# Kernel optimization log

Hardware: AMD Instinct MI355X
Metric: run time of the kernel (lower is better)

## Reference

```python
import jax, jax.numpy as jnp
import numpy as np

B, N, D_MODEL = 2, 2048, 1024
H, HEAD_DIM, D1 = 16, 128, 2048
NK, RANK = 16, 32
GAMMA = 0.999


def setup_inputs() -> dict:
    key = jax.random.key(0)
    ks = jax.random.split(key, 12)
    std = 0.02
    return {
        "x": jax.random.normal(ks[0], (B, N, D_MODEL), jnp.float32),
        "Wu": jax.random.normal(ks[1], (D_MODEL, D1), jnp.float32) * std,
        "bu": jax.random.normal(ks[2], (D1,), jnp.float32) * std,
        "Wv": jax.random.normal(ks[3], (D_MODEL, D1), jnp.float32) * std,
        "bv": jax.random.normal(ks[4], (D1,), jnp.float32) * std,
        "Wo": jax.random.normal(ks[5], (D1, D_MODEL), jnp.float32) * std,
        "bo": jax.random.normal(ks[6], (D_MODEL,), jnp.float32) * std,
        # SKI low-rank Toeplitz kernel factors at nk inducing relative positions
        "a_pos": jax.random.normal(ks[7], (H, NK, RANK), jnp.float32) * 0.1,
        "b_pos": jax.random.normal(ks[8], (H, RANK, HEAD_DIM), jnp.float32) * 0.1,
        "a_neg": jax.random.normal(ks[9], (H, NK, RANK), jnp.float32) * 0.1,
        "b_neg": jax.random.normal(ks[10], (H, RANK, HEAD_DIM), jnp.float32) * 0.1,
        "t_zero": jax.random.normal(ks[11], (H, HEAD_DIM), jnp.float32) * 0.1,
    }


def _interp_decay_kernel(a, b, n):
    # low-rank kernel at nk inducing points: [h, nk, d]
    k_ind = jnp.einsum("hkr,hrd->hkd", a, b)
    lags = jnp.arange(1, n)                      # lags 1..n-1
    p = (lags - 1.0) / (n - 2.0) * (NK - 1)      # map lag onto inducing grid
    lo = jnp.floor(p).astype(jnp.int32)
    hi = jnp.minimum(lo + 1, NK - 1)
    w = (p - lo)[None, :, None]
    k = k_ind[:, lo, :] * (1.0 - w) + k_ind[:, hi, :] * w  # [h, n-1, d]
    decay = (GAMMA ** lags)[None, :, None]
    return k * decay


def reference(x, Wu, bu, Wv, bv, Wo, bo, a_pos, b_pos, a_neg, b_neg, t_zero):
    u = jax.nn.silu(x @ Wu + bu)                 # [b, n, d1]
    v = jax.nn.silu(x @ Wv + bv)                 # [b, n, d1]
    n = v.shape[1]
    vh = v.reshape(v.shape[0], n, H, HEAD_DIM)   # [b, n, h, d]

    kp = _interp_decay_kernel(a_pos, b_pos, n)   # [h, n-1, d]
    kn = _interp_decay_kernel(a_neg, b_neg, n)   # [h, n-1, d]
    m = 2 * n
    k_full = jnp.zeros((H, m, HEAD_DIM), vh.dtype)
    k_full = k_full.at[:, 0].set(t_zero)
    k_full = k_full.at[:, 1:n].set(kp)
    k_full = k_full.at[:, m - jnp.arange(1, n)].set(kn)  # non-causal (negative lags)

    # circular FFT convolution along the sequence axis
    vf = jnp.fft.rfft(vh, n=m, axis=1)                    # [b, mf, h, d]
    kf = jnp.transpose(jnp.fft.rfft(k_full, axis=1), (1, 0, 2))[None]  # [1, mf, h, d]
    y = jnp.fft.irfft(vf * kf, n=m, axis=1)[:, :n]        # [b, n, h, d]

    out = u * y.reshape(y.shape[0], n, D1)                # elementwise gate
    return out @ Wo + bo
```

## Files before the change

### kernel.cpp

```cpp
#include <hip/hip_runtime.h>
#include <hip/hip_bf16.h>
#include <stdint.h>
#include <stddef.h>

#define BB 2
#define NSEQ 2048
#define DM 1024
#define H 16
#define HD 128
#define D1 2048
#define NKI 16
#define RANKI 32
#define MROWS (BB * NSEQ)
#define VPROWS 6144
#define NTAP 28
#define NPAIR 13
#define NCHUNK 128
#define CLEN 16
#define NSEG 16
#define SEGC (NCHUNK / NSEG)
#define GAMMA_F 0.999f
#define G_CL 0.9841201f
#define G_SC8 0.87979895f
#define LN_G (-1.00050033e-3f)

__device__ constexpr int TAPS[NTAP] = {
  1, 2, 138, 139, 274, 275, 411, 412, 547, 548, 684,
  820, 821, 956, 957, 1093, 1094, 1229, 1230, 1366,
  1502, 1503, 1638, 1639, 1775, 1776, 1911, 1912};
__device__ constexpr int LEADL[NPAIR] = {1, 138, 274, 411, 547, 820, 956, 1093, 1229, 1502, 1638, 1775, 1911};
__device__ constexpr int LEADI[NPAIR] = {0, 2, 4, 6, 8, 11, 13, 15, 17, 20, 22, 24, 26};
#define SGL0_L 684
#define SGL0_I 10
#define SGL1_L 1366
#define SGL1_I 19

typedef short short8 __attribute__((ext_vector_type(8)));
typedef float floatx4 __attribute__((ext_vector_type(4)));

__device__ __forceinline__ float bf2f(unsigned short u) {
  union { unsigned int i; float f; } v; v.i = ((unsigned int)u) << 16; return v.f;
}
__device__ __forceinline__ unsigned short f2bf(float f) {
  union { float f; unsigned int i; } v; v.f = f;
  unsigned int r = (v.i + 0x7FFFu + ((v.i >> 16) & 1u)) >> 16;
  return (unsigned short)r;
}
__device__ __forceinline__ float bflo(unsigned int p) {
  union { unsigned int i; float f; } v; v.i = p << 16; return v.f;
}
__device__ __forceinline__ float bfhi(unsigned int p) {
  union { unsigned int i; float f; } v; v.i = p & 0xffff0000u; return v.f;
}
__device__ __forceinline__ void async16(const unsigned short* g, unsigned short* l) {
  __builtin_amdgcn_global_load_lds(
      (const __attribute__((address_space(1))) unsigned int*)g,
      (__attribute__((address_space(3))) unsigned int*)l, 16, 0, 0);
}

#define CVT4 (MROWS * DM / 4)
__global__ __launch_bounds__(256) void prep_kernel(const float* __restrict__ x,
                                                   unsigned short* __restrict__ x_bf,
                                                   unsigned short* __restrict__ zrow) {
  int i = blockIdx.x * 256 + threadIdx.x;
  if (i < CVT4) {
    float4 f = ((const float4*)x)[i];
    ushort4 o;
    o.x = f2bf(f.x); o.y = f2bf(f.y); o.z = f2bf(f.z); o.w = f2bf(f.w);
    ((ushort4*)x_bf)[i] = o;
  } else {
    int j = i - CVT4;
    if (j < 256) {
      uint4 z; z.x = z.y = z.z = z.w = 0u;
      ((uint4*)zrow)[j] = z;
    }
  }
}

__device__ __forceinline__ float KinterpL(const float* kk, int l, int d) {
  if (l < 1) return 0.0f;
  float p = (float)(l - 1) * (15.0f / 2046.0f);
  int lo = (int)p; if (lo > 15) lo = 15;
  int hi = lo + 1; if (hi > 15) hi = 15;
  float w = p - (float)lo;
  float v = kk[lo * HD + d] * (1.0f - w) + kk[hi * HD + d] * w;
  return v * __powf(GAMMA_F, (float)l);
}

__global__ __launch_bounds__(256) void wprep_kernel(const float* __restrict__ Wu,
                                                    const float* __restrict__ Wv,
                                                    const float* __restrict__ Wo,
                                                    unsigned short* __restrict__ WT2,
                                                    unsigned short* __restrict__ WoT,
                                                    const float* __restrict__ ap,
                                                    const float* __restrict__ bp,
                                                    const float* __restrict__ an,
                                                    const float* __restrict__ bn,
                                                    float* __restrict__ dtp,
                                                    float* __restrict__ dtn) {
  int blk = blockIdx.x;
  int tid = threadIdx.x;
  if (blk < 6144) {
    __shared__ unsigned short t[32][33];
    const float* in; unsigned short* out;
    int rows, cols, bx, by;
    if (blk < 2048) {
      in = Wo; out = WoT; rows = D1; cols = DM;
      bx = (blk & 31) * 32; by = (blk >> 5) * 32;
    } else {
      int local = blk - 2048;
      int z = local >> 11, l2 = local & 2047;
      in = z ? Wv : Wu; out = WT2 + (size_t)z * D1 * DM;
      rows = DM; cols = D1;
      bx = (l2 & 63) * 32; by = (l2 >> 6) * 32;
    }
    int tx = tid & 31, ty = tid >> 5;
#pragma unroll
    for (int j = 0; j < 32; j += 8)
      t[ty + j][tx] = f2bf(in[(size_t)(by + ty + j) * cols + bx + tx]);
    __syncthreads();
#pragma unroll
    for (int j = 0; j < 32; j += 8)
      out[(size_t)(bx + ty + j) * rows + by + tx] = t[tx][ty + j];
  } else {
    __shared__ float kk[NKI * HD];
    int e0 = blk - 6144;
    int h = e0 & 15, dir = e0 >> 4;
    const float* a = (dir ? an : ap) + h * NKI * RANKI;
    const float* b = (dir ? bn : bp) + h * RANKI * HD;
    for (int e = tid; e < NKI * HD; e += 256) {
      int k = e >> 7, d = e & 127;
      float s = 0.0f;
#pragma unroll
      for (int r = 0; r < RANKI; ++r) s += a[k * RANKI + r] * b[r * HD + d];
      kk[e] = s;
    }
    __syncthreads();
    float* dt = (dir ? dtn : dtp) + (size_t)h * NTAP * HD;
    for (int e = tid; e < NTAP * HD; e += 256) {
      int j = e >> 7, d = e & 127;
      int l = TAPS[j];
      float K0 = KinterpL(kk, l, d);
      float K1 = KinterpL(kk, l - 1, d);
      float K2 = KinterpL(kk, l - 2, d);
      dt[e] = K0 - 2.0f * GAMMA_F * K1 + (GAMMA_F * GAMMA_F) * K2;
    }
  }
}

__global__ __launch_bounds__(512) void gemm_uv8(const unsigned short* __restrict__ A,
                                                const unsigned short* __restrict__ Bt,
                                                const float* __restrict__ bu,
                                                const float* __restrict__ bv,
                                                unsigned short* __restrict__ U,
                                                unsigned short* __restrict__ Vp) {
  __shared__ unsigned short lds[65536];
  constexpr int K = DM;
  constexpr int NT = K / 64;
  int lin = blockIdx.y * 16 + blockIdx.x;
  int swz = (lin & 7) * 32 + (lin >> 3);
  int n0 = (swz & 15) * 256;
  int m0 = (swz >> 4) * 256;
  int tid = threadIdx.x;
  int lane = tid & 63, w = tid >> 6;
  int wm = w >> 2, wn = w & 3;
  int q = lane >> 4, l16 = lane & 15;
  int srow = lane >> 3;
  int soff = ((lane & 7) ^ srow) << 3;
  const unsigned short* Ab = A + (size_t)(m0 + w * 8 + srow) * K + soff;
  const unsigned short* Bb = Bt + (size_t)(n0 + w * 8 + srow) * K + soff;
  unsigned aoff0 = w * 512;
  unsigned boff0 = 32768u + w * 512;
  int swk0 = (q ^ (l16 & 7)) << 3;
  int swk1 = ((4 | q) ^ (l16 & 7)) << 3;
  int pAr = wm * 8192;
  int pBr = 32768 + (wn >> 1) * 8192;
  int rB0 = (wn & 1) * 64;

  floatx4 acc[8][4];
#pragma unroll
  for (int f = 0; f < 8; ++f)
#pragma unroll
    for (int g = 0; g < 4; ++g) acc[f][g] = (floatx4){0.f, 0.f, 0.f, 0.f};

  auto stage = [&](int p, int t) {
    const unsigned short* a = Ab + t * 64;
    const unsigned short* b = Bb + t * 64;
    unsigned ao = aoff0 + p * 16384;
    unsigned bo = boff0 + p * 16384;
    async16(a,               &lds[ao]);
    async16(a + (size_t)64 * K,  &lds[ao + 4096]);
    async16(a + (size_t)128 * K, &lds[ao + 8192]);
    async16(a + (size_t)192 * K, &lds[ao + 12288]);
    async16(b,               &lds[bo]);
    async16(b + (size_t)64 * K,  &lds[bo + 4096]);
    async16(b + (size_t)128 * K, &lds[bo + 8192]);
    async16(b + (size_t)192 * K, &lds[bo + 12288]);
  };

  stage(0, 0);
  stage(1, 1);
  asm volatile("s_waitcnt vmcnt(8)" ::: "memory");
  __builtin_amdgcn_s_barrier();

  for (int t = 0; t < NT; ++t) {
    int p = t & 1;
    const unsigned short* As = &lds[pAr + p * 16384];
    const unsigned short* Bs = &lds[pBr + p * 16384];
    short8 bfr[4][2];
#pragma unroll
    for (int g = 0; g < 4; ++g) {
      int rh = (rB0 + g * 16 + l16) * 64;
      bfr[g][0] = *(const short8*)(Bs + rh + swk0);
      bfr[g][1] = *(const short8*)(Bs + rh + swk1);
    }
#pragma unroll
    for (int mh = 0; mh < 2; ++mh) {
      short8 af[4][2];
#pragma unroll
      for (int f = 0; f < 4; ++f) {
        int rh = ((mh * 4 + f) * 16 + l16) * 64;
        af[f][0] = *(const short8*)(As + rh + swk0);
        af[f][1] = *(const short8*)(As + rh + swk1);
      }
      __builtin_amdgcn_s_setprio(1);
#pragma unroll
      for (int f = 0; f < 4; ++f)
#pragma unroll
        for (int g = 0; g < 4; ++g) {
          acc[mh * 4 + f][g] = __builtin_amdgcn_mfma_f32_16x16x32_bf16(
              af[f][0], bfr[g][0], acc[mh * 4 + f][g], 0, 0, 0);
          acc[mh * 4 + f][g] = __builtin_amdgcn_mfma_f32_16x16x32_bf16(
              af[f][1], bfr[g][1], acc[mh * 4 + f][g], 0, 0, 0);
        }
      __builtin_amdgcn_s_setprio(0);
    }
    if (t == NT - 1) break;
    asm volatile("" ::: "memory");
    __builtin_amdgcn_s_barrier();
    if (t + 2 < NT) {
      stage(p, t + 2);
      asm volatile("s_waitcnt vmcnt(8)" ::: "memory");
    } else {
      asm volatile("s_waitcnt vmcnt(0)" ::: "memory");
    }
    __builtin_amdgcn_s_barrier();
  }

  int isv = (n0 >= 2048);
  const float* bias = isv ? bv : bu;
#pragma unroll
  for (int f = 0; f < 8; ++f) {
#pragma unroll
    for (int g = 0; g < 4; ++g) {
      int n = n0 + wn * 64 + g * 16 + l16;
      int nc = isv ? (n - 2048) : n;
      float bsv = bias[nc];
#pragma unroll
      for (int r = 0; r < 4; ++r) {
        int m = m0 + wm * 128 + f * 16 + q * 4 + r;
        float val = acc[f][g][r] + bsv;
        val = val / (1.0f + __expf(-val));
        if (isv) {
          size_t mrow = (size_t)(2048 + m + ((m >> 11) << 12));
          Vp[mrow * 2048 + nc] = f2bf(val);
        } else {
          U[(size_t)m * 2048 + nc] = f2bf(val);
        }
      }
    }
  }
}

__global__ __launch_bounds__(512) void gemm_out2(const unsigned short* __restrict__ A,
                                                 const unsigned short* __restrict__ Bt,
                                                 const float* __restrict__ bias,
                                                 float* __restrict__ C) {
  __shared__ unsigned short lds[32768];
  constexpr int K = D1;
  constexpr int NT = K / 64;
  int lin = blockIdx.y * 8 + blockIdx.x;
  int swz = (lin & 7) * 32 + (lin >> 3);
  int n0 = (swz & 7) * 128;
  int m0 = (swz >> 3) * 128;
  int tid = threadIdx.x;
  int lane = tid & 63, w = tid >> 6;
  int wm = w >> 1, wn = w & 1;
  int q = lane >> 4, l16 = lane & 15;
  int srow = lane >> 3;
  int soff = ((lane & 7) ^ srow) << 3;
  const unsigned short* Ab = A + (size_t)(m0 + w * 8 + srow) * K + soff;
  const unsigned short* Bb = Bt + (size_t)(n0 + w * 8 + srow) * K + soff;
  unsigned aoff0 = w * 512;
  unsigned boff0 = 16384u + w * 512;
  int swk0 = (q ^ (l16 & 7)) << 3;
  int swk1 = ((4 | q) ^ (l16 & 7)) << 3;

  floatx4 acc[2][4];
#pragma unroll
  for (int f = 0; f < 2; ++f)
#pragma unroll
    for (int g = 0; g < 4; ++g) acc[f][g] = (floatx4){0.f, 0.f, 0.f, 0.f};

  auto stage = [&](int p, int t) {
    const unsigned short* a = Ab + t * 64;
    const unsigned short* b = Bb + t * 64;
    unsigned ao = aoff0 + p * 8192;
    unsigned bo = boff0 + p * 8192;
    async16(a,                  &lds[ao]);
    async16(a + (size_t)64 * K, &lds[ao + 4096]);
    async16(b,                  &lds[bo]);
    async16(b + (size_t)64 * K, &lds[bo + 4096]);
  };

  stage(0, 0);
  stage(1, 1);
  asm volatile("s_waitcnt vmcnt(4)" ::: "memory");
  __builtin_amdgcn_s_barrier();

  for (int t = 0; t < NT; ++t) {
    int p = t & 1;
    const unsigned short* As = &lds[p * 8192];
    const unsigned short* Bs = &lds[16384 + p * 8192];
    short8 af[2][2], bfr[4][2];
#pragma unroll
    for (int g = 0; g < 4; ++g) {
      int rh = (wn * 64 + g * 16 + l16) * 64;
      bfr[g][0] = *(const short8*)(Bs + rh + swk0);
      bfr[g][1] = *(const short8*)(Bs + rh + swk1);
    }
#pragma unroll
    for (int f = 0; f < 2; ++f) {
      int rh = (wm * 32 + f * 16 + l16) * 64;
      af[f][0] = *(const short8*)(As + rh + swk0);
      af[f][1] = *(const short8*)(As + rh + swk1);
    }
    __builtin_amdgcn_s_setprio(1);
#pragma unroll
    for (int f = 0; f < 2; ++f)
#pragma unroll
      for (int g = 0; g < 4; ++g) {
        acc[f][g] = __builtin_amdgcn_mfma_f32_16x16x32_bf16(
            af[f][0], bfr[g][0], acc[f][g], 0, 0, 0);
        acc[f][g] = __builtin_amdgcn_mfma_f32_16x16x32_bf16(
            af[f][1], bfr[g][1], acc[f][g], 0, 0, 0);
      }
    __builtin_amdgcn_s_setprio(0);
    if (t == NT - 1) break;
    asm volatile("" ::: "memory");
    __builtin_amdgcn_s_barrier();
    if (t + 2 < NT) {
      stage(p, t + 2);
      asm volatile("s_waitcnt vmcnt(4)" ::: "memory");
    } else {
      asm volatile("s_waitcnt vmcnt(0)" ::: "memory");
    }
    __builtin_amdgcn_s_barrier();
  }

#pragma unroll
  for (int f = 0; f < 2; ++f) {
#pragma unroll
    for (int g = 0; g < 4; ++g) {
      int n = n0 + wn * 64 + g * 16 + l16;
      float bsv = bias[n];
#pragma unroll
      for (int r = 0; r < 4; ++r) {
        int m = m0 + wm * 32 + f * 16 + q * 4 + r;
        C[(size_t)m * DM + n] = acc[f][g][r] + bsv;
      }
    }
  }
}

__global__ __launch_bounds__(256, 1) void scan_chunks(const unsigned short* __restrict__ Vp,
                                                      const unsigned short* __restrict__ zr,
                                                      const float* __restrict__ dp,
                                                      const float* __restrict__ dn,
                                                      unsigned short* __restrict__ ypl,
                                                      unsigned short* __restrict__ ynl,
                                                      float* __restrict__ Sy_ex,
                                                      float* __restrict__ SG_ex) {
  int z = blockIdx.z;
  int dir = z >> 1, b = z & 1;
  int chunk = blockIdx.y;
  int c0 = blockIdx.x * 512 + threadIdx.x * 2;
  int h = c0 >> 7, d = c0 & 127;
  const float* dt = (dir ? dn : dp) + ((size_t)h * NTAP) * HD + d;
  float2 dreg[NTAP];
#pragma unroll
  for (int j = 0; j < NTAP; ++j) dreg[j] = *(const float2*)(dt + j * HD);
  const unsigned short* Vd = Vp + (size_t)b * VPROWS * D1 + (size_t)2048 * D1;
  unsigned short* yl = (dir ? ynl : ypl) + (size_t)b * NSEQ * D1 + c0;
  float sy0 = 0.f, sy1 = 0.f, sg0 = 0.f, sg1 = 0.f;
  float carry0[NPAIR], carry1[NPAIR];
  if (!dir) {
    int t0 = chunk * CLEN;
#pragma unroll
    for (int p = 0; p < NPAIR; ++p) {
      int tr = t0 - 1 - LEADL[p];
      const unsigned short* rb = (tr >= 0) ? (Vd + (size_t)tr * D1) : zr;
      unsigned int pk = *(const unsigned int*)(rb + c0);
      carry0[p] = bflo(pk); carry1[p] = bfhi(pk);
    }
    for (int i = 0; i < CLEN; ++i) {
      int t = t0 + i;
      float F0 = 0.f, F1 = 0.f;
#pragma unroll
      for (int p = 0; p < NPAIR; ++p) {
        int tr = t - LEADL[p];
        const unsigned short* rb = (tr >= 0) ? (Vd + (size_t)tr * D1) : zr;
        unsigned int pk = *(const unsigned int*)(rb + c0);
        float vl0 = bflo(pk), vl1 = bfhi(pk);
        F0 += dreg[LEADI[p]].x * vl0 + dreg[LEADI[p] + 1].x * carry0[p];
        F1 += dreg[LEADI[p]].y * vl1 + dreg[LEADI[p] + 1].y * carry1[p];
        carry0[p] = vl0; carry1[p] = vl1;
      }
      {
        int tr = t - SGL0_L;
        const unsigned short* rb = (tr >= 0) ? (Vd + (size_t)tr * D1) : zr;
        unsigned int pk = *(const unsigned int*)(rb + c0);
        F0 += dreg[SGL0_I].x * bflo(pk); F1 += dreg[SGL0_I].y * bfhi(pk);
      }
      {
        int tr = t - SGL1_L;
        const unsigned short* rb = (tr >= 0) ? (Vd + (size_t)tr * D1) : zr;
        unsigned int pk = *(const unsigned int*)(rb + c0);
        F0 += dreg[SGL1_I].x * bflo(pk); F1 += dreg[SGL1_I].y * bfhi(pk);
      }
      sg0 = GAMMA_F * sg0 + F0; sy0 = GAMMA_F * sy0 + sg0;
      sg1 = GAMMA_F * sg1 + F1; sy1 = GAMMA_F * sy1 + sg1;
      unsigned int pack = (unsigned int)f2bf(sy0) | ((unsigned int)f2bf(sy1) << 16);
      *(unsigned int*)(yl + (size_t)t * D1) = pack;
    }
  } else {
    int tstart = (NSEQ - 1) - chunk * CLEN;
#pragma unroll
    for (int p = 0; p < NPAIR; ++p) {
      int tr = tstart + 1 + LEADL[p];
      const unsigned short* rb = (tr <= NSEQ - 1) ? (Vd + (size_t)tr * D1) : zr;
      unsigned int pk = *(const unsigned int*)(rb + c0);
      carry0[p] = bflo(pk); carry1[p] = bfhi(pk);
    }
    for (int i = 0; i < CLEN; ++i) {
      int t = tstart - i;
      float F0 = 0.f, F1 = 0.f;
#pragma unroll
      for (int p = 0; p < NPAIR; ++p) {
        int tr = t + LEADL[p];
        const unsigned short* rb = (tr <= NSEQ - 1) ? (Vd + (size_t)tr * D1) : zr;
        unsigned int pk = *(const unsigned int*)(rb + c0);
        float vl0 = bflo(pk), vl1 = bfhi(pk);
        F0 += dreg[LEADI[p]].x * vl0 + dreg[LEADI[p] + 1].x * carry0[p];
        F1 += dreg[LEADI[p]].y * vl1 + dreg[LEADI[p] + 1].y * carry1[p];
        carry0[p] = vl0; carry1[p] = vl1;
      }
      {
        int tr = t + SGL0_L;
        const unsigned short* rb = (tr <= NSEQ - 1) ? (Vd + (size_t)tr * D1) : zr;
        unsigned int pk = *(const unsigned int*)(rb + c0);
        F0 += dreg[SGL0_I].x * bflo(pk); F1 += dreg[SGL0_I].y * bfhi(pk);
      }
      {
        int tr = t + SGL1_L;
        const unsigned short* rb = (tr <= NSEQ - 1) ? (Vd + (size_t)tr * D1) : zr;
        unsigned int pk = *(const unsigned int*)(rb + c0);
        F0 += dreg[SGL1_I].x * bflo(pk); F1 += dreg[SGL1_I].y * bfhi(pk);
      }
      sg0 = GAMMA_F * sg0 + F0; sy0 = GAMMA_F * sy0 + sg0;
      sg1 = GAMMA_F * sg1 + F1; sy1 = GAMMA_F * sy1 + sg1;
      unsigned int pack = (unsigned int)f2bf(sy0) | ((unsigned int)f2bf(sy1) << 16);
      *(unsigned int*)(yl + (size_t)t * D1) = pack;
    }
  }
  size_t sidx = ((size_t)z * NCHUNK + chunk) * D1 + c0;
  Sy_ex[sidx] = sy0; Sy_ex[sidx + 1] = sy1;
  SG_ex[sidx] = sg0; SG_ex[sidx + 1] = sg1;
}

__global__ __launch_bounds__(256) void state_scan2(const float* __restrict__ Sy_ex,
                                                   const float* __restrict__ SG_ex,
                                                   float* __restrict__ Sy_in,
                                                   float* __restrict__ SG_in,
                                                   float* __restrict__ Xy,
                                                   float* __restrict__ Xg) {
  int idx = blockIdx.x * 256 + threadIdx.x;
  int c = idx & (D1 - 1);
  int zs = idx >> 11;
  int z = zs >> 4, seg = zs & (NSEG - 1);
  float ey = 0.f, eg = 0.f;
#pragma unroll
  for (int m = 0; m < SEGC; ++m) {
    int k = seg * SEGC + m;
    size_t s = ((size_t)z * NCHUNK + k) * D1 + c;
    Sy_in[s] = ey; SG_in[s] = eg;
    float lex = Sy_ex[s], lgx = SG_ex[s];
    ey = lex + G_CL * (ey + (float)CLEN * eg);
    eg = lgx + G_CL * eg;
  }
  size_t xi = (size_t)zs * D1 + c;
  Xy[xi] = ey; Xg[xi] = eg;
}

__global__ __launch_bounds__(256) void seg_scan(const float* __restrict__ Xy,
                                                const float* __restrict__ Xg,
                                                float* __restrict__ Ey,
                                                float* __restrict__ Eg) {
  int idx = blockIdx.x * 256 + threadIdx.x;
  int z = idx >> 11, c = idx & (D1 - 1);
  float ey = 0.f, eg = 0.f;
#pragma unroll
  for (int s = 0; s < NSEG; ++s) {
    size_t xi = ((size_t)z * NSEG + s) * D1 + c;
    Ey[xi] = ey; Eg[xi] = eg;
    float xy = Xy[xi], xg = Xg[xi];
    ey = xy + G_SC8 * (ey + 128.0f * eg);
    eg = xg + G_SC8 * eg;
  }
}

__global__ __launch_bounds__(256) void combine_kernel(const unsigned short* __restrict__ ypl,
                                                      const unsigned short* __restrict__ ynl,
                                                      const unsigned short* __restrict__ Vp,
                                                      const float* __restrict__ Sy_in,
                                                      const float* __restrict__ SG_in,
                                                      const float* __restrict__ Ey,
                                                      const float* __restrict__ Eg,
                                                      const float* __restrict__ tz,
                                                      const unsigned short* __restrict__ U,
                                                      unsigned short* __restrict__ G) {
  int e = blockIdx.x * 256 + threadIdx.x;
  int cq = e & (D1 / 4 - 1);
  int c0 = cq * 4;
  int r = e >> 9;
  int t = r & (NSEQ - 1);
  int b = r >> 11;
  int kp = t >> 4;  float dpD = (float)((t & 15) + 1);
  int tau = (NSEQ - 1) - t;
  int kn = tau >> 4; float dnD = (float)((tau & 15) + 1);
  float gp = __expf(dpD * LN_G);
  float gn = __expf(dnD * LN_G);
  size_t ix = (size_t)r * D1 + c0;
  size_t sp = ((size_t)(b) * NCHUNK + kp) * D1 + c0;
  size_t sn = ((size_t)(2 + b) * NCHUNK + kn) * D1 + c0;
  uint2 pyl = *(const uint2*)(ypl + ix);
  uint2 pyn = *(const uint2*)(ynl + ix);
  uint2 pv  = *(const uint2*)(Vp + ((size_t)b * VPROWS + 2048 + t) * D1 + c0);
  uint2 pu  = *(const uint2*)(U + ix);
  float4 syp = *(const float4*)(Sy_in + sp);
  float4 sgp = *(const float4*)(SG_in + sp);
  float4 syn = *(const float4*)(Sy_in + sn);
  float4 sgn = *(const float4*)(SG_in + sn);
  float4 tzv = *(const float4*)(tz + c0);
  int mp = kp & (SEGC - 1), mn = kn & (SEGC - 1);
  size_t ep = ((size_t)b * NSEG + (kp >> 3)) * D1 + c0;
  size_t en = ((size_t)(2 + b) * NSEG + (kn >> 3)) * D1 + c0;
  float4 eyp = *(const float4*)(Ey + ep);
  float4 egp = *(const float4*)(Eg + ep);
  float4 eyn = *(const float4*)(Ey + en);
  float4 egn = *(const float4*)(Eg + en);
  float gmp = __expf((float)(CLEN * mp) * LN_G);
  float gmn = __expf((float)(CLEN * mn) * LN_G);
  float cmp = 16.0f * (float)mp, cmn = 16.0f * (float)mn;
  syp.x += gmp * (eyp.x + cmp * egp.x); sgp.x += gmp * egp.x;
  syp.y += gmp * (eyp.y + cmp * egp.y); sgp.y += gmp * egp.y;
  syp.z += gmp * (eyp.z + cmp * egp.z); sgp.z += gmp * egp.z;
  syp.w += gmp * (eyp.w + cmp * egp.w); sgp.w += gmp * egp.w;
  syn.x += gmn * (eyn.x + cmn * egn.x); sgn.x += gmn * egn.x;
  syn.y += gmn * (eyn.y + cmn * egn.y); sgn.y += gmn * egn.y;
  syn.z += gmn * (eyn.z + cmn * egn.z); sgn.z += gmn * egn.z;
  syn.w += gmn * (eyn.w + cmn * egn.w); sgn.w += gmn * egn.w;
  float yv[4], uv[4], vv[4];
  yv[0] = bflo(pyl.x) + gp * (syp.x + dpD * sgp.x) + bflo(pyn.x) + gn * (syn.x + dnD * sgn.x);
  yv[1] = bfhi(pyl.x) + gp * (syp.y + dpD * sgp.y) + bfhi(pyn.x) + gn * (syn.y + dnD * sgn.y);
  yv[2] = bflo(pyl.y) + gp * (syp.z + dpD * sgp.z) + bflo(pyn.y) + gn * (syn.z + dnD * sgn.z);
  yv[3] = bfhi(pyl.y) + gp * (syp.w + dpD * sgp.w) + bfhi(pyn.y) + gn * (syn.w + dnD * sgn.w);
  vv[0] = bflo(pv.x); vv[1] = bfhi(pv.x); vv[2] = bflo(pv.y); vv[3] = bfhi(pv.y);
  uv[0] = bflo(pu.x); uv[1] = bfhi(pu.x); uv[2] = bflo(pu.y); uv[3] = bfhi(pu.y);
  float tza[4] = {tzv.x, tzv.y, tzv.z, tzv.w};
  uint2 og;
  unsigned short g0 = f2bf(uv[0] * (yv[0] + tza[0] * vv[0]));
  unsigned short g1 = f2bf(uv[1] * (yv[1] + tza[1] * vv[1]));
  unsigned short g2 = f2bf(uv[2] * (yv[2] + tza[2] * vv[2]));
  unsigned short g3 = f2bf(uv[3] * (yv[3] + tza[3] * vv[3]));
  og.x = (unsigned int)g0 | ((unsigned int)g1 << 16);
  og.y = (unsigned int)g2 | ((unsigned int)g3 << 16);
  *(uint2*)(G + ix) = og;
}

extern "C" void kernel_launch(void* const* d_in, const int* in_sizes, int n_in,
                              void* d_out, int out_size, void* d_ws, size_t ws_size,
                              hipStream_t stream) {
  const float* x      = (const float*)d_in[0];
  const float* Wu     = (const float*)d_in[1];
  const float* bu     = (const float*)d_in[2];
  const float* Wv     = (const float*)d_in[3];
  const float* bv     = (const float*)d_in[4];
  const float* Wo     = (const float*)d_in[5];
  const float* bo     = (const float*)d_in[6];
  const float* a_pos  = (const float*)d_in[7];
  const float* b_pos  = (const float*)d_in[8];
  const float* a_neg  = (const float*)d_in[9];
  const float* b_neg  = (const float*)d_in[10];
  const float* t_zero = (const float*)d_in[11];
  float* out = (float*)d_out;

  char* ws = (char*)d_ws;
  unsigned short* x_bf  = (unsigned short*)ws; ws += (size_t)MROWS * DM * 2;
  unsigned short* u_ws  = (unsigned short*)ws; ws += (size_t)MROWS * D1 * 2;
  unsigned short* Vp    = (unsigned short*)ws; ws += (size_t)BB * VPROWS * D1 * 2;
  unsigned short* ypl   = (unsigned short*)ws; ws += (size_t)MROWS * D1 * 2;
  unsigned short* ynl   = (unsigned short*)ws; ws += (size_t)MROWS * D1 * 2;
  unsigned short* WoT   = (unsigned short*)ws; ws += (size_t)DM * D1 * 2;
  float* dtp   = (float*)ws; ws += (size_t)H * NTAP * HD * 4;
  float* dtn   = (float*)ws; ws += (size_t)H * NTAP * HD * 4;
  float* Sy_in = (float*)ws; ws += (size_t)4 * NCHUNK * D1 * 4;
  float* SG_in = (float*)ws; ws += (size_t)4 * NCHUNK * D1 * 4;
  unsigned short* zrow = (unsigned short*)ws; ws += (size_t)D1 * 2;
  float* Xy = (float*)ws; ws += (size_t)4 * NSEG * D1 * 4;
  float* Xg = (float*)ws; ws += (size_t)4 * NSEG * D1 * 4;
  float* Ey = (float*)ws; ws += (size_t)4 * NSEG * D1 * 4;
  float* Eg = (float*)ws; ws += (size_t)4 * NSEG * D1 * 4;
  float* Sy_ex = (float*)x_bf;
  float* SG_ex = (float*)x_bf + (size_t)4 * NCHUNK * D1;
  unsigned short* WT2 = ypl;

  dim3 tb256(256);
  prep_kernel<<<dim3(CVT4 / 256 + 1), tb256, 0, stream>>>(x, x_bf, zrow);
  wprep_kernel<<<dim3(6176), tb256, 0, stream>>>(
      Wu, Wv, Wo, WT2, WoT, a_pos, b_pos, a_neg, b_neg, dtp, dtn);
  gemm_uv8<<<dim3(16, 16), dim3(512), 0, stream>>>(x_bf, WT2, bu, bv, u_ws, Vp);
  scan_chunks<<<dim3(D1 / 512, NCHUNK, 4), tb256, 0, stream>>>(Vp, zrow, dtp, dtn, ypl, ynl, Sy_ex, SG_ex);
  state_scan2<<<dim3(4 * NSEG * D1 / 256), tb256, 0, stream>>>(Sy_ex, SG_ex, Sy_in, SG_in, Xy, Xg);
  seg_scan<<<dim3(4 * D1 / 256), tb256, 0, stream>>>(Xy, Xg, Ey, Eg);
  combine_kernel<<<dim3((size_t)MROWS * D1 / 1024), tb256, 0, stream>>>(
      ypl, ynl, Vp, Sy_in, SG_in, Ey, Eg, t_zero, u_ws, u_ws);
  gemm_out2<<<dim3(8, 32), dim3(512), 0, stream>>>(u_ws, WoT, bo, out);
}
```

Measured before the change: 253.2 us.

## Retile UV GEMM to 256x128 blocks with triple-buffered LDS pipeline

Changes the fused U/V projection GEMM from 256x256 tiles on 256 blocks to 256x128 tiles on 512 blocks, so each wave computes a 64x64 sub-tile. Replaces the two-stage double buffer with a three-stage LDS ring that needs one barrier per K step, and interleaves the next stage's async global loads between the two halves of the MFMA work. The aim is better CU occupancy and load/compute overlap. In exchange there is less operand reuse per block, more total global traffic, and a larger LDS footprint.

```diff
diff --git a/kernel.cpp b/kernel.cpp
--- a/kernel.cpp
+++ b/kernel.cpp
@@ -148,109 +148,111 @@
   }
 }
 
-__global__ __launch_bounds__(512) void gemm_uv8(const unsigned short* __restrict__ A,
-                                                const unsigned short* __restrict__ Bt,
-                                                const float* __restrict__ bu,
-                                                const float* __restrict__ bv,
-                                                unsigned short* __restrict__ U,
-                                                unsigned short* __restrict__ Vp) {
-  __shared__ unsigned short lds[65536];
+__global__ __launch_bounds__(512) void gemm_uvr3(const unsigned short* __restrict__ A,
+                                                 const unsigned short* __restrict__ Bt,
+                                                 const float* __restrict__ bu,
+                                                 const float* __restrict__ bv,
+                                                 unsigned short* __restrict__ U,
+                                                 unsigned short* __restrict__ Vp) {
+  __shared__ unsigned short lds[73728];
   constexpr int K = DM;
   constexpr int NT = K / 64;
-  int lin = blockIdx.y * 16 + blockIdx.x;
-  int swz = (lin & 7) * 32 + (lin >> 3);
-  int n0 = (swz & 15) * 256;
-  int m0 = (swz >> 4) * 256;
+  int lin = blockIdx.y * 32 + blockIdx.x;
+  int swz = (lin & 7) * 64 + (lin >> 3);
+  int n0 = (swz & 31) * 128;
+  int m0 = (swz >> 5) * 256;
   int tid = threadIdx.x;
   int lane = tid & 63, w = tid >> 6;
-  int wm = w >> 2, wn = w & 3;
+  int wm = w >> 1, wn = w & 1;
   int q = lane >> 4, l16 = lane & 15;
   int srow = lane >> 3;
   int soff = ((lane & 7) ^ srow) << 3;
   const unsigned short* Ab = A + (size_t)(m0 + w * 8 + srow) * K + soff;
   const unsigned short* Bb = Bt + (size_t)(n0 + w * 8 + srow) * K + soff;
-  unsigned aoff0 = w * 512;
-  unsigned boff0 = 32768u + w * 512;
+  unsigned wl = w * 512;
   int swk0 = (q ^ (l16 & 7)) << 3;
   int swk1 = ((4 | q) ^ (l16 & 7)) << 3;
-  int pAr = wm * 8192;
-  int pBr = 32768 + (wn >> 1) * 8192;
-  int rB0 = (wn & 1) * 64;
-
-  floatx4 acc[8][4];
-#pragma unroll
-  for (int f = 0; f < 8; ++f)
+  int rdA = wm * 4096 + l16 * 64;
+  int rdB = 16384 + wn * 4096 + l16 * 64;
+
+  floatx4 acc[4][4];
+#pragma unroll
+  for (int f = 0; f < 4; ++f)
 #pragma unroll
     for (int g = 0; g < 4; ++g) acc[f][g] = (floatx4){0.f, 0.f, 0.f, 0.f};
 
-  auto stage = [&](int p, int t) {
-    const unsigned short* a = Ab + t * 64;
-    const unsigned short* b = Bb + t * 64;
-    unsigned ao = aoff0 + p * 16384;
-    unsigned bo = boff0 + p * 16384;
-    async16(a,               &lds[ao]);
-    async16(a + (size_t)64 * K,  &lds[ao + 4096]);
-    async16(a + (size_t)128 * K, &lds[ao + 8192]);
-    async16(a + (size_t)192 * K, &lds[ao + 12288]);
-    async16(b,               &lds[bo]);
-    async16(b + (size_t)64 * K,  &lds[bo + 4096]);
-    async16(b + (size_t)128 * K, &lds[bo + 8192]);
-    async16(b + (size_t)192 * K, &lds[bo + 12288]);
+  auto stageA = [&](int s, int t, int c) {
+    async16(Ab + ((size_t)c * 64) * K + t * 64, &lds[s * 24576 + c * 4096 + wl]);
   };
-
-  stage(0, 0);
-  stage(1, 1);
-  asm volatile("s_waitcnt vmcnt(8)" ::: "memory");
-  __builtin_amdgcn_s_barrier();
+  auto stageB = [&](int s, int t, int c) {
+    async16(Bb + ((size_t)c * 64) * K + t * 64, &lds[s * 24576 + 16384 + c * 4096 + wl]);
+  };
+
+  stageA(0, 0, 0); stageA(0, 0, 1); stageA(0, 0, 2); stageA(0, 0, 3);
+  stageB(0, 0, 0); stageB(0, 0, 1);
+  stageA(1, 1, 0); stageA(1, 1, 1); stageA(1, 1, 2); stageA(1, 1, 3);
+  stageB(1, 1, 0); stageB(1, 1, 1);
 
   for (int t = 0; t < NT; ++t) {
-    int p = t & 1;
-    const unsigned short* As = &lds[pAr + p * 16384];
-    const unsigned short* Bs = &lds[pBr + p * 16384];
+    int s = t % 3;
+    int s2 = (t + 2) % 3;
+    if (t == NT - 1) {
+      asm volatile("s_waitcnt vmcnt(0)" ::: "memory");
+    } else {
+      asm volatile("s_waitcnt vmcnt(6)" ::: "memory");
+    }
+    __builtin_amdgcn_s_barrier();
+    asm volatile("" ::: "memory");
+    const unsigned short* L = &lds[s * 24576];
+    int st = (t + 2 < NT);
+    if (st) { stageA(s2, t + 2, 0); stageA(s2, t + 2, 1); stageA(s2, t + 2, 2); }
     short8 bfr[4][2];
 #pragma unroll
     for (int g = 0; g < 4; ++g) {
-      int rh = (rB0 + g * 16 + l16) * 64;
-      bfr[g][0] = *(const short8*)(Bs + rh + swk0);
-      bfr[g][1] = *(const short8*)(Bs + rh + swk1);
-    }
-#pragma unroll
-    for (int mh = 0; mh < 2; ++mh) {
-      short8 af[4][2];
-#pragma unroll
-      for (int f = 0; f < 4; ++f) {
-        int rh = ((mh * 4 + f) * 16 + l16) * 64;
-        af[f][0] = *(const short8*)(As + rh + swk0);
-        af[f][1] = *(const short8*)(As + rh + swk1);
-      }
-      __builtin_amdgcn_s_setprio(1);
-#pragma unroll
-      for (int f = 0; f < 4; ++f)
-#pragma unroll
-        for (int g = 0; g < 4; ++g) {
-          acc[mh * 4 + f][g] = __builtin_amdgcn_mfma_f32_16x16x32_bf16(
-              af[f][0], bfr[g][0], acc[mh * 4 + f][g], 0, 0, 0);
-          acc[mh * 4 + f][g] = __builtin_amdgcn_mfma_f32_16x16x32_bf16(
-              af[f][1], bfr[g][1], acc[mh * 4 + f][g], 0, 0, 0);
-        }
-      __builtin_amdgcn_s_setprio(0);
-    }
-    if (t == NT - 1) break;
-    asm volatile("" ::: "memory");
-    __builtin_amdgcn_s_barrier();
-    if (t + 2 < NT) {
-      stage(p, t + 2);
-      asm volatile("s_waitcnt vmcnt(8)" ::: "memory");
-    } else {
-      asm volatile("s_waitcnt vmcnt(0)" ::: "memory");
-    }
-    __builtin_amdgcn_s_barrier();
+      bfr[g][0] = *(const short8*)(L + rdB + g * 1024 + swk0);
+      bfr[g][1] = *(const short8*)(L + rdB + g * 1024 + swk1);
+    }
+    short8 af0[2][2];
+#pragma unroll
+    for (int f = 0; f < 2; ++f) {
+      af0[f][0] = *(const short8*)(L + rdA + f * 1024 + swk0);
+      af0[f][1] = *(const short8*)(L + rdA + f * 1024 + swk1);
+    }
+    __builtin_amdgcn_s_setprio(1);
+#pragma unroll
+    for (int f = 0; f < 2; ++f)
+#pragma unroll
+      for (int g = 0; g < 4; ++g) {
+        acc[f][g] = __builtin_amdgcn_mfma_f32_16x16x32_bf16(
+            af0[f][0], bfr[g][0], acc[f][g], 0, 0, 0);
+        acc[f][g] = __builtin_amdgcn_mfma_f32_16x16x32_bf16(
+            af0[f][1], bfr[g][1], acc[f][g], 0, 0, 0);
+      }
+    __builtin_amdgcn_s_setprio(0);
+    if (st) { stageA(s2, t + 2, 3); stageB(s2, t + 2, 0); stageB(s2, t + 2, 1); }
+    short8 af1[2][2];
+#pragma unroll
+    for (int f = 0; f < 2; ++f) {
+      af1[f][0] = *(const short8*)(L + rdA + (2 + f) * 1024 + swk0);
+      af1[f][1] = *(const short8*)(L + rdA + (2 + f) * 1024 + swk1);
+    }
+    __builtin_amdgcn_s_setprio(1);
+#pragma unroll
+    for (int f = 0; f < 2; ++f)
+#pragma unroll
+      for (int g = 0; g < 4; ++g) {
+        acc[2 + f][g] = __builtin_amdgcn_mfma_f32_16x16x32_bf16(
+            af1[f][0], bfr[g][0], acc[2 + f][g], 0, 0, 0);
+        acc[2 + f][g] = __builtin_amdgcn_mfma_f32_16x16x32_bf16(
+            af1[f][1], bfr[g][1], acc[2 + f][g], 0, 0, 0);
+      }
+    __builtin_amdgcn_s_setprio(0);
   }
 
   int isv = (n0 >= 2048);
   const float* bias = isv ? bv : bu;
 #pragma unroll
-  for (int f = 0; f < 8; ++f) {
+  for (int f = 0; f < 4; ++f) {
 #pragma unroll
     for (int g = 0; g < 4; ++g) {
       int n = n0 + wn * 64 + g * 16 + l16;
@@ -258,7 +260,7 @@
       float bsv = bias[nc];
 #pragma unroll
       for (int r = 0; r < 4; ++r) {
-        int m = m0 + wm * 128 + f * 16 + q * 4 + r;
+        int m = m0 + wm * 64 + f * 16 + q * 4 + r;
         float val = acc[f][g][r] + bsv;
         val = val / (1.0f + __expf(-val));
         if (isv) {
@@ -629,7 +631,7 @@
   prep_kernel<<<dim3(CVT4 / 256 + 1), tb256, 0, stream>>>(x, x_bf, zrow);
   wprep_kernel<<<dim3(6176), tb256, 0, stream>>>(
       Wu, Wv, Wo, WT2, WoT, a_pos, b_pos, a_neg, b_neg, dtp, dtn);
-  gemm_uv8<<<dim3(16, 16), dim3(512), 0, stream>>>(x_bf, WT2, bu, bv, u_ws, Vp);
+  gemm_uvr3<<<dim3(32, 16), dim3(512), 0, stream>>>(x_bf, WT2, bu, bv, u_ws, Vp);
   scan_chunks<<<dim3(D1 / 512, NCHUNK, 4), tb256, 0, stream>>>(Vp, zrow, dtp, dtn, ypl, ynl, Sy_ex, SG_ex);
   state_scan2<<<dim3(4 * NSEG * D1 / 256), tb256, 0, stream>>>(Sy_ex, SG_ex, Sy_in, SG_in, Xy, Xg);
   seg_scan<<<dim3(4 * D1 / 256), tb256, 0, stream>>>(Xy, Xg, Ey, Eg);
```

Result: slower. 259.6 us (+2.6%).
